# Kernel tuning notes

Hardware: AMD Instinct MI355X
Metric: run time of the kernel (lower is better)

The kernel has to match this reference:

```python
import jax, jax.numpy as jnp
import numpy as np

BN_EPS = 1e-5
ALPHA = 0.5


def setup_inputs() -> dict:
    key = jax.random.key(0)
    ks = jax.random.split(key, 12)
    N, F, D, L, E = 8192, 256, 256, 3, 262144
    s = 1.0 / np.sqrt(D)
    return {
        "x": jax.random.normal(ks[0], (N, F), jnp.float32),
        "edge_index": jax.random.randint(ks[1], (2, E), 0, N, jnp.int64),
        "latent": jax.random.normal(ks[2], (N, D), jnp.float32),
        "adj_changes": jax.random.normal(ks[3], (N, N), jnp.float32) * 0.01,
        "feature_change": jax.random.normal(ks[4], (F, F), jnp.float32) * s,
        "ft_W": jax.random.normal(ks[5], (D, F), jnp.float32) * s,
        "ft_b": jax.random.normal(ks[6], (D,), jnp.float32) * 0.01,
        "gnn_W": jax.random.normal(ks[7], (L, D, D), jnp.float32) * s,
        "gnn_b": jax.random.normal(ks[8], (L, D), jnp.float32) * 0.01,
        "bn_gamma": jnp.ones((L, D), jnp.float32),
        "bn_beta": jnp.zeros((L, D), jnp.float32),
        "mlp_W": jax.random.normal(ks[9], (1, D), jnp.float32) * s,
        "mlp_b": jax.random.normal(ks[10], (1,), jnp.float32) * 0.01,
    }


def reference(x, edge_index, latent, adj_changes, feature_change, ft_W, ft_b,
              gnn_W, gnn_b, bn_gamma, bn_beta, mlp_W, mlp_b):
    N = x.shape[0]
    L = gnn_W.shape[0]
    src, dst = edge_index[0], edge_index[1]
    # to_dense_adj: dense binary adjacency [N, N]
    adj = jnp.zeros((N, N), x.dtype).at[src, dst].set(1.0)
    # get_modified_adj: zero the diagonal of adj_changes, clamp to [-1, 1], add adj
    acs = adj_changes - jnp.diag(jnp.diag(adj_changes))
    acs = jnp.clip(acs, -1.0, 1.0)
    modified_adj = acs + adj
    # dense_to_sparse + GINConv ignores edge weights -> binarized adjacency
    A_bin = (modified_adj != 0).astype(x.dtype)  # non-differentiable mask, as in torch

    x_orig = x
    h = x @ feature_change          # [N, F]
    h = h @ ft_W.T + ft_b           # [N, D]
    for l in range(L):
        # GINConv (eps=0): mlp(x_i + sum over source neighbors) ; flow src->dst => A^T @ h
        agg = A_bin.T @ h
        h = (agg + h) @ gnn_W[l].T + gnn_b[l]
        # BatchNorm1d (training mode: biased batch statistics)
        mean = jnp.mean(h, axis=0)
        var = jnp.var(h, axis=0)
        h = (h - mean) * jax.lax.rsqrt(var + BN_EPS) * bn_gamma[l] + bn_beta[l]
        # dropout(p=0) is identity
        h = jax.nn.relu(h)
    out = jax.nn.sigmoid(h @ mlp_W.T + mlp_b)  # [N, 1]

    # loss_func: per-node reconstruction score
    attr_err = jnp.sqrt(jnp.sum((out - x_orig) ** 2, axis=1))          # broadcast [N,F]
    struct_err = jnp.sqrt(jnp.sum((modified_adj - adj) ** 2, axis=1))  # [N]
    score = ALPHA * attr_err + (1.0 - ALPHA) * struct_err
    return out, jnp.mean(score)
```

## Files before the change

kernel.cpp:

```cpp
#include <hip/hip_runtime.h>

constexpr int N = 8192;
constexpr int D = 256;
constexpr int E = 262144;
constexpr float BN_EPS = 1e-5f;
constexpr int SCAP = 128;
constexpr int QCAP = 256;
constexpr int RCAP = 8;
constexpr int ZOCAP = 128;


__global__ __launch_bounds__(256) void k_scan_r10(
    const float* __restrict__ ac, const float* __restrict__ x,
    const unsigned int* __restrict__ ei32,
    float* __restrict__ sterr, float* __restrict__ xrs, float* __restrict__ xrss,
    int* __restrict__ candcnt, int* __restrict__ cand,
    int* __restrict__ selfloop, int* __restrict__ found, int* __restrict__ flags)
{
    int b = blockIdx.x, tid = threadIdx.x;
    if (tid < 4) selfloop[b * 4 + tid] = 0;
    if (b == 1 && tid < QCAP) found[tid] = 0;
    if (b == 0 && tid == 0) {
        unsigned int acc2 = 0;
        for (int k = 0; k < 8; ++k) acc2 |= ei32[2 * k + 1];
        for (int f = 0; f < 8; ++f) flags[f] = 0;
        flags[2] = (acc2 == 0u) ? 1 : 0;
    }
    __shared__ int lcnt;
    __shared__ float part[3][4];

    for (int r = 0; r < 4; ++r) {
        int i = b * 4 + r;
        if (tid == 0) lcnt = 0;
        __syncthreads();
        const float* row = ac + (size_t)i * N;
        float ss = 0.f;
        #pragma unroll
        for (int p = 0; p < 8; ++p) {
            int j = p * 1024 + tid * 4;
            float4 v = *reinterpret_cast<const float4*>(row + j);
            float a0 = fminf(fmaxf(v.x, -1.f), 1.f);
            float a1 = fminf(fmaxf(v.y, -1.f), 1.f);
            float a2 = fminf(fmaxf(v.z, -1.f), 1.f);
            float a3 = fminf(fmaxf(v.w, -1.f), 1.f);
            ss += a0 * a0; ss += a1 * a1; ss += a2 * a2; ss += a3 * a3;
            bool pr = (v.x == 0.f) | (v.x <= -1.f) |
                      (v.y == 0.f) | (v.y <= -1.f) |
                      (v.z == 0.f) | (v.z <= -1.f) |
                      (v.w == 0.f) | (v.w <= -1.f);
            if (__ballot(pr)) {
                #pragma unroll
                for (int c = 0; c < 4; ++c) {
                    float a = (&v.x)[c];
                    int jj = j + c;
                    if (jj != i && (a == 0.f || a <= -1.f)) {
                        int pos = atomicAdd(&lcnt, 1);
                        if (pos < RCAP) cand[i * RCAP + pos] = (jj << 1) | ((a <= -1.f) ? 1 : 0);
                    }
                }
            }
        }
        float xv = x[(size_t)i * 256 + tid];
        float xs = xv, xq = xv * xv;
        #pragma unroll
        for (int s2 = 32; s2 > 0; s2 >>= 1) {
            ss += __shfl_xor(ss, s2);
            xs += __shfl_xor(xs, s2);
            xq += __shfl_xor(xq, s2);
        }
        int wv = tid >> 6, ln = tid & 63;
        if (ln == 0) { part[0][wv] = ss; part[1][wv] = xs; part[2][wv] = xq; }
        __syncthreads();
        if (tid == 0) {
            float St = part[0][0] + part[0][1] + part[0][2] + part[0][3];
            float dgn = fminf(fmaxf(row[i], -1.f), 1.f);
            sterr[i] = sqrtf(fmaxf(St - dgn * dgn, 0.f));
            xrs[i]  = part[1][0] + part[1][1] + part[1][2] + part[1][3];
            xrss[i] = part[2][0] + part[2][1] + part[2][2] + part[2][3];
            candcnt[i] = (lcnt < RCAP) ? lcnt : RCAP;
        }
        __syncthreads();
    }
}

__device__ __forceinline__ int build_qlist(const int* __restrict__ candcnt,
                                           const int* __restrict__ cand,
                                           int2* ql, int* cs )
{
    int t = threadIdx.x, base = t * 32;
    int c = 0;
    for (int r = base; r < base + 32; ++r) c += candcnt[r];
    cs[t] = c;
    __syncthreads();
    if (t == 0) {
        int o = 0;
        for (int i2 = 0; i2 < 256; ++i2) { int v = cs[i2]; cs[i2] = o; o += v; }
        cs[256] = (o < QCAP) ? o : QCAP;
    }
    __syncthreads();
    int p = cs[t];
    for (int r = base; r < base + 32; ++r) {
        int cnt = candcnt[r];
        for (int q = 0; q < cnt; ++q) {
            if (p < QCAP) { int enc = cand[r * RCAP + q]; ql[p] = make_int2(r, enc); }
            p++;
        }
    }
    __syncthreads();
    return cs[256];
}

__global__ __launch_bounds__(256) void k_edges_r10(
    const void* __restrict__ ei, const int* __restrict__ flags,
    const int* __restrict__ candcnt, const int* __restrict__ cand,
    int* __restrict__ selfloop, int* __restrict__ found)
{
    __shared__ int2 ql[QCAP];
    __shared__ int cs[257];
    int nq = build_qlist(candcnt, cand, ql, cs);
    int tid = threadIdx.x;
    int mode = flags[2];
    #pragma unroll
    for (int e2 = 0; e2 < 2; ++e2) {
        int k = blockIdx.x * 512 + e2 * 256 + tid;
        int s, d;
        if (mode) { const long long* p = (const long long*)ei; s = (int)p[k]; d = (int)p[E + k]; }
        else      { const int* p = (const int*)ei; s = p[k]; d = p[E + k]; }
        if (s == d && (unsigned)s < (unsigned)N) selfloop[s] = 1;
        for (int q = 0; q < nq; ++q)
            if (s == ql[q].x && d == (ql[q].y >> 1)) found[q] = 1;
    }
}

struct SpecSet { int ns, nz; };
__device__ __forceinline__ SpecSet build_special(
    const int* __restrict__ candcnt, const int* __restrict__ cand,
    const int* __restrict__ found, const int* __restrict__ selfloop,
    unsigned char* spf , int* spidx , int2* zofl ,
    int2* ql , int* cs , int* misc )
{
    int nq = build_qlist(candcnt, cand, ql, cs);
    int t = threadIdx.x, base = t * 32;
    for (int r = base; r < base + 32; ++r) spf[r] = (unsigned char)selfloop[r];
    __syncthreads();
    if (t == 0) {
        int nz = 0;
        for (int q = 0; q < nq; ++q) {
            int2 cd = ql[q];
            int col = cd.y >> 1, neg = cd.y & 1;
            int zero = neg ? found[q] : !found[q];
            if (zero && nz < ZOCAP) { zofl[nz] = make_int2(cd.x, col); spf[col] = 1; nz++; }
        }
        misc[1] = nz;
    }
    __syncthreads();
    int c = 0;
    for (int r = base; r < base + 32; ++r) c += spf[r];
    cs[t] = c;
    __syncthreads();
    if (t == 0) {
        int o = 0;
        for (int i2 = 0; i2 < 256; ++i2) { int v = cs[i2]; cs[i2] = o; o += v; }
        misc[0] = (o < SCAP) ? o : SCAP;
    }
    __syncthreads();
    int p = cs[t];
    for (int r = base; r < base + 32; ++r)
        if (spf[r]) { if (p < SCAP) spidx[p] = r; p++; }
    __syncthreads();
    SpecSet ss; ss.ns = misc[0]; ss.nz = misc[1];
    return ss;
}

__device__ __forceinline__ float h0_row(
    const float* __restrict__ x, const float* __restrict__ fc,
    const float* __restrict__ ftW, const float* __restrict__ ftb,
    int row, float* xr, float* Ts)
{
    int d = threadIdx.x;
    xr[d] = x[(size_t)row * 256 + d];
    __syncthreads();
    float tacc = 0.f;
    for (int k = 0; k < 256; ++k) tacc += xr[k] * fc[k * 256 + d];
    Ts[d] = tacc;
    __syncthreads();
    float h = ftb[d];
    const float4* w4 = reinterpret_cast<const float4*>(ftW + (size_t)d * 256);
    const float4* t4 = reinterpret_cast<const float4*>(Ts);
    for (int k = 0; k < 64; ++k) {
        float4 a = t4[k], b = w4[k];
        h += a.x * b.x + a.y * b.y + a.z * b.z + a.w * b.w;
    }
    __syncthreads();
    return h;
}

__global__ __launch_bounds__(256) void k_L0_r10(
    const float* __restrict__ x, const float* __restrict__ fc,
    const float* __restrict__ ftW, const float* __restrict__ ftb,
    const float* __restrict__ gnnW0,
    const int* __restrict__ candcnt, const int* __restrict__ cand,
    const int* __restrict__ found, const int* __restrict__ selfloop,
    int* __restrict__ flags, int* __restrict__ sppos_g, int* __restrict__ spidx_g,
    int2* __restrict__ zoff_g,
    float* __restrict__ DP0)
{
    __shared__ unsigned char spf[N];
    __shared__ int2 ql[QCAP];
    __shared__ int cs[257];
    __shared__ int misc[2];
    __shared__ int2 zofl[ZOCAP];
    __shared__ int spidx[SCAP];
    __shared__ float xr[256], Ts[256], Dl[256];

    SpecSet ss = build_special(candcnt, cand, found, selfloop,
                               spf, spidx, zofl, ql, cs, misc);
    int j = blockIdx.x, t = threadIdx.x;

    if (j == 0) {
        int p = cs[t], base = t * 32;
        for (int r = base; r < base + 32; ++r) {
            sppos_g[r] = spf[r] ? ((p < SCAP) ? p : -1) : -1;
            p += spf[r];
        }
        if (t < SCAP) spidx_g[t] = (t < ss.ns) ? spidx[t] : -1;
        if (t < ZOCAP && t < ss.nz) zoff_g[t] = zofl[t];
        if (t == 0) { flags[4] = ss.ns; flags[1] = ss.nz; }
    }
    if (j >= ss.ns) return;

    int row = spidx[j];
    float delta = 0.f;
    if (selfloop[row]) delta = h0_row(x, fc, ftW, ftb, row, xr, Ts);
    for (int z = 0; z < ss.nz; ++z) {
        if (zofl[z].y == row) {
            __syncthreads();
            delta -= h0_row(x, fc, ftW, ftb, zofl[z].x, xr, Ts);
        }
    }
    Dl[t] = delta;
    __syncthreads();
    const float4* w4 = reinterpret_cast<const float4*>(gnnW0 + (size_t)t * 256);
    const float4* d4 = reinterpret_cast<const float4*>(Dl);
    float acc = 0.f;
    for (int k = 0; k < 64; ++k) {
        float4 a = d4[k], b = w4[k];
        acc += a.x * b.x + a.y * b.y + a.z * b.z + a.w * b.w;
    }
    DP0[j * 256 + t] = acc;
}

__global__ __launch_bounds__(256) void k_layer_r10(
    const float* __restrict__ prevDP, const float* __restrict__ gnnWl,
    const float* __restrict__ gammaPrev, const float* __restrict__ betaPrev,
    const int* __restrict__ flags,
    const int* __restrict__ spidx, const int* __restrict__ sppos,
    const int* __restrict__ selfloop, const int2* __restrict__ zoff,
    float* __restrict__ curDP)
{
    int j = blockIdx.x;
    int ns = flags[4];
    if (j >= ns) return;
    int d = threadIdx.x;
    int row = spidx[j];
    int nz = flags[1];
    __shared__ float Dl[256];
    float sum = 0.f;
    for (int jj = 0; jj < ns; ++jj) sum += prevDP[jj * 256 + d];
    float cbar = sum / (float)N;
    float var = (float)(N - ns) * cbar * cbar;
    for (int jj = 0; jj < ns; ++jj) { float u = prevDP[jj * 256 + d] - cbar; var += u * u; }
    var /= (float)N;
    float sc = gammaPrev[d] * rsqrtf(var + BN_EPS);
    float b = betaPrev[d];
    float delta = 0.f;
    if (selfloop[row]) delta = fmaxf((prevDP[j * 256 + d] - cbar) * sc + b, 0.f);
    for (int z = 0; z < nz; ++z) {
        if (zoff[z].y == row) {
            int s = zoff[z].x, sp = sppos[s];
            float y = (sp >= 0) ? fmaxf((prevDP[sp * 256 + d] - cbar) * sc + b, 0.f)
                                : fmaxf(b - cbar * sc, 0.f);
            delta -= y;
        }
    }
    Dl[d] = delta;
    __syncthreads();
    const float4* w4 = reinterpret_cast<const float4*>(gnnWl + (size_t)d * 256);
    const float4* d4 = reinterpret_cast<const float4*>(Dl);
    float acc = 0.f;
    for (int k = 0; k < 64; ++k) {
        float4 a = d4[k], b2 = w4[k];
        acc += a.x * b2.x + a.y * b2.y + a.z * b2.z + a.w * b2.w;
    }
    curDP[j * 256 + d] = acc;
}

__global__ __launch_bounds__(1024) void k_final_r10(
    const float* __restrict__ DP2,
    const float* __restrict__ gamma2, const float* __restrict__ beta2,
    const float* __restrict__ mlpW, const float* __restrict__ mlpb,
    const int* __restrict__ flags, const int* __restrict__ sppos,
    const float* __restrict__ xrs, const float* __restrict__ xrss,
    const float* __restrict__ sterr,
    float* __restrict__ out)
{
    int t = threadIdx.x;
    int ns = flags[4];
    __shared__ float cb[256], sc[256], bt[256];
    __shared__ float os[SCAP + 1];
    if (t < 256) {
        int d = t;
        float sum = 0.f;
        for (int jj = 0; jj < ns; ++jj) sum += DP2[jj * 256 + d];
        float cbar = sum / (float)N;
        float var = (float)(N - ns) * cbar * cbar;
        for (int jj = 0; jj < ns; ++jj) { float u = DP2[jj * 256 + d] - cbar; var += u * u; }
        var /= (float)N;
        cb[d] = cbar;
        sc[d] = gamma2[d] * rsqrtf(var + BN_EPS);
        bt[d] = beta2[d];
    }
    __syncthreads();
    int wave = t >> 6, lane = t & 63;
    for (int j = wave; j <= ns; j += 16) {
        float part = 0.f;
        #pragma unroll
        for (int q = 0; q < 4; ++q) {
            int d = lane + q * 64;
            float y = (j < ns) ? fmaxf((DP2[j * 256 + d] - cb[d]) * sc[d] + bt[d], 0.f)
                               : fmaxf(bt[d] - cb[d] * sc[d], 0.f);
            part += y * mlpW[d];
        }
        #pragma unroll
        for (int s2 = 32; s2 > 0; s2 >>= 1) part += __shfl_xor(part, s2);
        if (lane == 0) os[j] = 1.f / (1.f + expf(-(part + mlpb[0])));
    }
    __syncthreads();
    float obase = os[ns];
    float psum = 0.f;
    for (int it = 0; it < N / 1024; ++it) {
        int r = it * 1024 + t;
        int sp = sppos[r];
        float o = (sp >= 0) ? os[sp] : obase;
        float attr = sqrtf(fmaxf(256.f * o * o - 2.f * o * xrs[r] + xrss[r], 0.f));
        out[r] = o;
        psum += 0.5f * attr + 0.5f * sterr[r];
    }
    __shared__ float red[1024];
    red[t] = psum;
    __syncthreads();
    for (int s2 = 512; s2 > 0; s2 >>= 1) {
        if (t < s2) red[t] += red[t + s2];
        __syncthreads();
    }
    if (t == 0) out[N] = red[0] / (float)N;
}

extern "C" void kernel_launch(void* const* d_in, const int* in_sizes, int n_in,
                              void* d_out, int out_size, void* d_ws, size_t ws_size,
                              hipStream_t stream) {
    const float* x     = (const float*)d_in[0];
    const void*  ei    = d_in[1];
    const float* ac    = (const float*)d_in[3];
    const float* fc    = (const float*)d_in[4];
    const float* ftW   = (const float*)d_in[5];
    const float* ftb   = (const float*)d_in[6];
    const float* gnnW  = (const float*)d_in[7];
    const float* gamma = (const float*)d_in[9];
    const float* beta  = (const float*)d_in[10];
    const float* mlpW  = (const float*)d_in[11];
    const float* mlpb  = (const float*)d_in[12];

    const size_t KB = 1u << 10;
    char* w = (char*)d_ws;
    float* sterr  = (float*)(w);
    float* xrs    = (float*)(w + 32 * KB);
    float* xrss   = (float*)(w + 64 * KB);
    int* candcnt  = (int*)  (w + 96 * KB);
    int* selfloop = (int*)  (w + 128 * KB);
    int* sppos    = (int*)  (w + 160 * KB);
    int* cand     = (int*)  (w + 192 * KB);
    int* found    = (int*)  (w + 448 * KB);
    int* flags    = (int*)  (w + 449 * KB);
    int2* zoff    = (int2*) (w + 450 * KB);
    int* spidx    = (int*)  (w + 451 * KB);
    float* DPa    = (float*)(w + 452 * KB);
    float* DPb    = (float*)(w + 580 * KB);

    float* out = (float*)d_out;

    k_scan_r10<<<N / 4, 256, 0, stream>>>(ac, x, (const unsigned int*)ei,
                                          sterr, xrs, xrss, candcnt, cand,
                                          selfloop, found, flags);
    k_edges_r10<<<E / 512, 256, 0, stream>>>(ei, flags, candcnt, cand, selfloop, found);
    k_L0_r10<<<SCAP, 256, 0, stream>>>(x, fc, ftW, ftb, gnnW + 0 * 65536,
                                       candcnt, cand, found, selfloop,
                                       flags, sppos, spidx, zoff, DPa);
    k_layer_r10<<<SCAP, 256, 0, stream>>>(DPa, gnnW + 1 * 65536, gamma, beta,
                                          flags, spidx, sppos, selfloop, zoff, DPb);
    k_layer_r10<<<SCAP, 256, 0, stream>>>(DPb, gnnW + 2 * 65536, gamma + 256, beta + 256,
                                          flags, spidx, sppos, selfloop, zoff, DPa);
    k_final_r10<<<1, 1024, 0, stream>>>(DPa, gamma + 512, beta + 512,
                                        mlpW, mlpb, flags, sppos, xrs, xrss, sterr, out);
}
```

Measured before the change: 167.6 us.

## Assign one wavefront per adjacency row in scan kernel, removing block syncs

Result: faster. 153.7 us (-8.3%).

```diff
diff --git a/kernel.cpp b/kernel.cpp
--- a/kernel.cpp
+++ b/kernel.cpp
@@ -10,7 +10,7 @@
 constexpr int ZOCAP = 128;
 
 
-__global__ __launch_bounds__(256) void k_scan_r10(
+__global__ __launch_bounds__(256) void k_scan_r11(
     const float* __restrict__ ac, const float* __restrict__ x,
     const unsigned int* __restrict__ ei32,
     float* __restrict__ sterr, float* __restrict__ xrs, float* __restrict__ xrss,
@@ -18,7 +18,9 @@
     int* __restrict__ selfloop, int* __restrict__ found, int* __restrict__ flags)
 {
     int b = blockIdx.x, tid = threadIdx.x;
-    if (tid < 4) selfloop[b * 4 + tid] = 0;
+    int wv = tid >> 6, lane = tid & 63;
+    int i = b * 4 + wv;
+
     if (b == 1 && tid < QCAP) found[tid] = 0;
     if (b == 0 && tid == 0) {
         unsigned int acc2 = 0;
@@ -26,60 +28,69 @@
         for (int f = 0; f < 8; ++f) flags[f] = 0;
         flags[2] = (acc2 == 0u) ? 1 : 0;
     }
-    __shared__ int lcnt;
-    __shared__ float part[3][4];
-
-    for (int r = 0; r < 4; ++r) {
-        int i = b * 4 + r;
-        if (tid == 0) lcnt = 0;
-        __syncthreads();
-        const float* row = ac + (size_t)i * N;
-        float ss = 0.f;
+    if (lane == 0) selfloop[i] = 0;
+
+    const float4* rp = reinterpret_cast<const float4*>(ac + (size_t)i * N);
+    float ss = 0.f;
+    int basecnt = 0;
+    unsigned long long lmask = (lane == 63) ? ~0ull >> 1 : (1ull << (lane + 1)) - 1ull;
+    lmask >>= 1;
+    lmask = (lane == 0) ? 0ull : (~0ull >> (64 - lane));
+
+    #pragma unroll
+    for (int u = 0; u < 4; ++u) {
+        float4 v[8];
         #pragma unroll
-        for (int p = 0; p < 8; ++p) {
-            int j = p * 1024 + tid * 4;
-            float4 v = *reinterpret_cast<const float4*>(row + j);
-            float a0 = fminf(fmaxf(v.x, -1.f), 1.f);
-            float a1 = fminf(fmaxf(v.y, -1.f), 1.f);
-            float a2 = fminf(fmaxf(v.z, -1.f), 1.f);
-            float a3 = fminf(fmaxf(v.w, -1.f), 1.f);
-            ss += a0 * a0; ss += a1 * a1; ss += a2 * a2; ss += a3 * a3;
-            bool pr = (v.x == 0.f) | (v.x <= -1.f) |
-                      (v.y == 0.f) | (v.y <= -1.f) |
-                      (v.z == 0.f) | (v.z <= -1.f) |
-                      (v.w == 0.f) | (v.w <= -1.f);
-            if (__ballot(pr)) {
+        for (int k = 0; k < 8; ++k) v[k] = rp[(u * 8 + k) * 64 + lane];
+        float minv = 1.f;
+        #pragma unroll
+        for (int k = 0; k < 8; ++k) {
+            float a0 = fminf(fmaxf(v[k].x, -1.f), 1.f);
+            float a1 = fminf(fmaxf(v[k].y, -1.f), 1.f);
+            float a2 = fminf(fmaxf(v[k].z, -1.f), 1.f);
+            float a3 = fminf(fmaxf(v[k].w, -1.f), 1.f);
+            ss = fmaf(a0, a0, ss); ss = fmaf(a1, a1, ss);
+            ss = fmaf(a2, a2, ss); ss = fmaf(a3, a3, ss);
+            float t0 = fabsf(fmaf(a0, a0, a0));
+            float t1 = fabsf(fmaf(a1, a1, a1));
+            float t2 = fabsf(fmaf(a2, a2, a2));
+            float t3 = fabsf(fmaf(a3, a3, a3));
+            minv = fminf(minv, fminf(fminf(t0, t1), fminf(t2, t3)));
+        }
+        if (__ballot(minv == 0.f)) {
+            #pragma unroll
+            for (int k = 0; k < 8; ++k) {
                 #pragma unroll
                 for (int c = 0; c < 4; ++c) {
-                    float a = (&v.x)[c];
-                    int jj = j + c;
-                    if (jj != i && (a == 0.f || a <= -1.f)) {
-                        int pos = atomicAdd(&lcnt, 1);
-                        if (pos < RCAP) cand[i * RCAP + pos] = (jj << 1) | ((a <= -1.f) ? 1 : 0);
+                    float a = (&v[k].x)[c];
+                    float acs = fminf(fmaxf(a, -1.f), 1.f);
+                    int jj = (u * 8 + k) * 256 + lane * 4 + c;
+                    bool pred = (fmaf(acs, acs, acs) == 0.f) && (jj != i);
+                    unsigned long long m = __ballot(pred);
+                    if (pred) {
+                        int slot = basecnt + __popcll(m & lmask);
+                        if (slot < RCAP)
+                            cand[i * RCAP + slot] = (jj << 1) | ((acs <= -1.f) ? 1 : 0);
                     }
+                    basecnt += (int)__popcll(m);
                 }
             }
         }
-        float xv = x[(size_t)i * 256 + tid];
-        float xs = xv, xq = xv * xv;
-        #pragma unroll
-        for (int s2 = 32; s2 > 0; s2 >>= 1) {
-            ss += __shfl_xor(ss, s2);
-            xs += __shfl_xor(xs, s2);
-            xq += __shfl_xor(xq, s2);
-        }
-        int wv = tid >> 6, ln = tid & 63;
-        if (ln == 0) { part[0][wv] = ss; part[1][wv] = xs; part[2][wv] = xq; }
-        __syncthreads();
-        if (tid == 0) {
-            float St = part[0][0] + part[0][1] + part[0][2] + part[0][3];
-            float dgn = fminf(fmaxf(row[i], -1.f), 1.f);
-            sterr[i] = sqrtf(fmaxf(St - dgn * dgn, 0.f));
-            xrs[i]  = part[1][0] + part[1][1] + part[1][2] + part[1][3];
-            xrss[i] = part[2][0] + part[2][1] + part[2][2] + part[2][3];
-            candcnt[i] = (lcnt < RCAP) ? lcnt : RCAP;
-        }
-        __syncthreads();
+    }
+    float4 xv = *reinterpret_cast<const float4*>(x + (size_t)i * 256 + lane * 4);
+    float xs = xv.x + xv.y + xv.z + xv.w;
+    float xq = xv.x * xv.x + xv.y * xv.y + xv.z * xv.z + xv.w * xv.w;
+    #pragma unroll
+    for (int s2 = 32; s2 > 0; s2 >>= 1) {
+        ss += __shfl_xor(ss, s2);
+        xs += __shfl_xor(xs, s2);
+        xq += __shfl_xor(xq, s2);
+    }
+    if (lane == 0) {
+        float dgn = fminf(fmaxf(ac[(size_t)i * N + i], -1.f), 1.f);
+        sterr[i] = sqrtf(fmaxf(ss - dgn * dgn, 0.f));
+        xrs[i] = xs; xrss[i] = xq;
+        candcnt[i] = (basecnt < RCAP) ? basecnt : RCAP;
     }
 }
 
@@ -110,7 +121,7 @@
     return cs[256];
 }
 
-__global__ __launch_bounds__(256) void k_edges_r10(
+__global__ __launch_bounds__(256) void k_edges_r11(
     const void* __restrict__ ei, const int* __restrict__ flags,
     const int* __restrict__ candcnt, const int* __restrict__ cand,
     int* __restrict__ selfloop, int* __restrict__ found)
@@ -195,7 +206,7 @@
     return h;
 }
 
-__global__ __launch_bounds__(256) void k_L0_r10(
+__global__ __launch_bounds__(256) void k_L0_r11(
     const float* __restrict__ x, const float* __restrict__ fc,
     const float* __restrict__ ftW, const float* __restrict__ ftb,
     const float* __restrict__ gnnW0,
@@ -250,7 +261,7 @@
     DP0[j * 256 + t] = acc;
 }
 
-__global__ __launch_bounds__(256) void k_layer_r10(
+__global__ __launch_bounds__(256) void k_layer_r11(
     const float* __restrict__ prevDP, const float* __restrict__ gnnWl,
     const float* __restrict__ gammaPrev, const float* __restrict__ betaPrev,
     const int* __restrict__ flags,
@@ -295,7 +306,7 @@
     curDP[j * 256 + d] = acc;
 }
 
-__global__ __launch_bounds__(1024) void k_final_r10(
+__global__ __launch_bounds__(1024) void k_final_r11(
     const float* __restrict__ DP2,
     const float* __restrict__ gamma2, const float* __restrict__ beta2,
     const float* __restrict__ mlpW, const float* __restrict__ mlpb,
@@ -389,17 +400,17 @@
 
     float* out = (float*)d_out;
 
-    k_scan_r10<<<N / 4, 256, 0, stream>>>(ac, x, (const unsigned int*)ei,
+    k_scan_r11<<<N / 4, 256, 0, stream>>>(ac, x, (const unsigned int*)ei,
                                           sterr, xrs, xrss, candcnt, cand,
                                           selfloop, found, flags);
-    k_edges_r10<<<E / 512, 256, 0, stream>>>(ei, flags, candcnt, cand, selfloop, found);
-    k_L0_r10<<<SCAP, 256, 0, stream>>>(x, fc, ftW, ftb, gnnW + 0 * 65536,
+    k_edges_r11<<<E / 512, 256, 0, stream>>>(ei, flags, candcnt, cand, selfloop, found);
+    k_L0_r11<<<SCAP, 256, 0, stream>>>(x, fc, ftW, ftb, gnnW + 0 * 65536,
                                        candcnt, cand, found, selfloop,
                                        flags, sppos, spidx, zoff, DPa);
-    k_layer_r10<<<SCAP, 256, 0, stream>>>(DPa, gnnW + 1 * 65536, gamma, beta,
+    k_layer_r11<<<SCAP, 256, 0, stream>>>(DPa, gnnW + 1 * 65536, gamma, beta,
                                           flags, spidx, sppos, selfloop, zoff, DPb);
-    k_layer_r10<<<SCAP, 256, 0, stream>>>(DPb, gnnW + 2 * 65536, gamma + 256, beta + 256,
+    k_layer_r11<<<SCAP, 256, 0, stream>>>(DPb, gnnW + 2 * 65536, gamma + 256, beta + 256,
                                           flags, spidx, sppos, selfloop, zoff, DPa);
-    k_final_r10<<<1, 1024, 0, stream>>>(DPa, gamma + 512, beta + 512,
+    k_final_r11<<<1, 1024, 0, stream>>>(DPa, gamma + 512, beta + 512,
                                         mlpW, mlpb, flags, sppos, xrs, xrss, sterr, out);
 }
```
